# Kernel tuning notes

Hardware: AMD Instinct MI355X
Metric: run time of the kernel (lower is better)

The kernel has to match this reference:

```python
import math
import jax, jax.numpy as jnp
import numpy as np

NUM_HEADS = 8
EMBED_DIM = 512   # embed_dim_per_head(64) * num_heads(8)
LATENT = 256
HIDDEN = 512
INPUT_DIM = 128
P = 3             # function 'Q' -> 3 polynomial coefficients


def setup_inputs() -> dict:
    key = jax.random.key(0)
    ks = jax.random.split(key, 16)
    B, L, T, D, E = 64, 2048, 1024, INPUT_DIM, EMBED_DIM
    s = lambda fan_in: 1.0 / math.sqrt(fan_in)
    inp = {
        "timesteps": jax.random.uniform(ks[0], (B, L), jnp.float32),
        "X": jax.random.normal(ks[1], (B, L, D), jnp.float32),
        "M": jax.random.bernoulli(ks[2], 0.5, (B, L, D)).astype(jnp.float32),
        "y_time_steps": jax.random.uniform(ks[3], (B, T), jnp.float32),
        # time_embedding: Linear(1, E)
        "w_te": jax.random.normal(ks[4], (E,), jnp.float32),
        "b_te": jnp.zeros((E,), jnp.float32),
        # learned query [1, P, E]
        "query": jax.random.normal(ks[5], (1, P, E), jnp.float32),
        # query_map / key_map: Linear(E, E), stored [in, out]
        "W_q": jax.random.normal(ks[6], (E, E), jnp.float32) * s(E),
        "b_q": jnp.zeros((E,), jnp.float32),
        "W_k": jax.random.normal(ks[7], (E, E), jnp.float32) * s(E),
        "b_k": jnp.zeros((E,), jnp.float32),
        # attn out: Linear(2*D*H, latent)
        "W_o": jax.random.normal(ks[8], (2 * D * NUM_HEADS, LATENT), jnp.float32) * s(2 * D * NUM_HEADS),
        "b_o": jnp.zeros((LATENT,), jnp.float32),
        # decoder MLP: latent -> hidden -> hidden -> D
        "W1": jax.random.normal(ks[9], (LATENT, HIDDEN), jnp.float32) * s(LATENT),
        "b1": jnp.zeros((HIDDEN,), jnp.float32),
        "W2": jax.random.normal(ks[10], (HIDDEN, HIDDEN), jnp.float32) * s(HIDDEN),
        "b2": jnp.zeros((HIDDEN,), jnp.float32),
        "W3": jax.random.normal(ks[11], (HIDDEN, D), jnp.float32) * s(HIDDEN),
        "b3": jnp.zeros((D,), jnp.float32),
    }
    return inp


def _fld_forward(timesteps, X, M, y_time_steps, w_te, b_te, query,
                 W_q, b_q, W_k, b_k, W_o, b_o, W1, b1, W2, b2, W3, b3):
    B, L = timesteps.shape
    D = X.shape[-1]
    E, H = EMBED_DIM, NUM_HEADS
    ek = E // H
    # learn_time_embedding: Linear(1,E) then sin on indices range(0, E, H)
    key = timesteps[..., None] * w_te + b_te                      # [B,L,E]
    sin_mask = (jnp.arange(E) % H) == 0
    key = jnp.where(sin_mask, jnp.sin(key), key)
    Xcat = jnp.concatenate([X, M], axis=-1)                       # [B,L,2D]
    Mcat = jnp.concatenate([M, M], axis=-1)                       # [B,L,2D]
    # mask is used only for masked_fill in torch (no grad through it)
    maskb = jax.lax.stop_gradient((Mcat != 0).astype(Xcat.dtype))
    q = jnp.broadcast_to(query, (B, P, E)) @ W_q + b_q            # [B,P,E]
    k = key @ W_k + b_k                                            # [B,L,E]
    qh = q.reshape(B, P, H, ek).transpose(0, 2, 1, 3)             # [B,H,P,ek]
    kh = k.reshape(B, L, H, ek).transpose(0, 2, 1, 3)             # [B,H,L,ek]
    scores = jnp.einsum('bhpe,bhle->bhpl', qh, kh) / math.sqrt(ek)
    # per-channel masked softmax over L, factorized (masked entries -> exp(-1e9)=0)
    m = jnp.max(scores, axis=-1, keepdims=True)
    w = jnp.exp(scores - m)                                        # [B,H,P,L]
    num = jnp.einsum('bhpl,blc->bhpc', w, maskb * Xcat)            # [B,H,P,2D]
    den = jnp.einsum('bhpl,blc->bhpc', w, maskb)
    x = num / den                                                  # [B,H,P,2D]
    x = x.transpose(0, 2, 1, 3).reshape(B, P, H * 2 * D)
    coeffs = x @ W_o + b_o                                         # [B,P,latent]
    t = y_time_steps[..., None]                                    # [B,T,1]
    c0 = coeffs[:, 0:1, :]
    c1 = coeffs[:, 1:2, :]
    c2 = coeffs[:, 2:3, :]
    z = c0 + t * c1 + (t * t) * c2                                 # [B,T,latent]
    h1 = jax.nn.relu(z @ W1 + b1)
    h2 = jax.nn.relu(h1 @ W2 + b2)
    return h2 @ W3 + b3                                            # [B,T,D]


def reference(timesteps, X, M, y_time_steps, w_te, b_te, query,
              W_q, b_q, W_k, b_k, W_o, b_o, W1, b1, W2, b2, W3, b3):
    return _fld_forward(timesteps, X, M, y_time_steps, w_te, b_te, query,
                        W_q, b_q, W_k, b_k, W_o, b_o, W1, b1, W2, b2, W3, b3)
```

## Files before the change

### kernel.cpp

```cpp
#include <hip/hip_runtime.h>
#include <math.h>

#define NH   8
#define PP   3
#define HP   24
#define E    512
#define EK   64
#define D    128
#define LL   2048
#define BB   64
#define TT   1024
#define LAT  256
#define HID  512
#define CH2  16

typedef __attribute__((ext_vector_type(8))) short bf16x8;
typedef __attribute__((ext_vector_type(16))) float f32x16;

#define OFF_VS     ((size_t)2048)
#define OFF_WA     ((size_t)4096)
#define OFF_WB     ((size_t)4128)
#define OFF_SB     ((size_t)4160)
#define OFF_CVP    ((size_t)73728)
#define OFF_P2     ((size_t)81920)
#define OFF_PART   ((size_t)475136)
#define OFF_SC     ((size_t)3620864)
#define OFF_A      ((size_t)3784704)

__device__ inline ushort f2bf(float x) {
    union { float f; uint u; } v; v.f = x;
    uint r = v.u + 0x7fffu + ((v.u >> 16) & 1u);
    return (ushort)(r >> 16);
}
__device__ inline float bf2f(ushort u) {
    union { uint u; float f; } v; v.u = (uint)u << 16;
    return v.f;
}
__device__ inline uint swz(uint a)  { return a ^ (((a >> 8) & 7u) << 4); }
__device__ inline uint swzH(uint a) { return a ^ (((a >> 7) & 7u) << 4); }
__device__ inline uint pk2(float lo, float hi) {
    return (uint)f2bf(lo) | ((uint)f2bf(hi) << 16);
}
__device__ inline float h1f(float a0, float a1, float a2, float t) {
    return fmaxf(fmaf(t, fmaf(t, a2, a1), a0), 0.f);
}
__device__ inline int sigma(int s) { return s ^ (((((s >> 2) ^ (s >> 3)) & 1)) ? 12 : 0); }

__global__ __launch_bounds__(512) void k_setup(const float* __restrict__ query,
                                               const float* __restrict__ W_q,
                                               const float* __restrict__ b_q,
                                               const float* __restrict__ W_k,
                                               const float* __restrict__ b_k,
                                               const float* __restrict__ w_te,
                                               const float* __restrict__ b_te,
                                               const float* __restrict__ W_o,
                                               const float* __restrict__ W2,
                                               const float* __restrict__ W3,
                                               float* __restrict__ vsin,
                                               float* __restrict__ wA,
                                               float* __restrict__ wB,
                                               float* __restrict__ sbias,
                                               float* __restrict__ cvp,
                                               ushort* __restrict__ W2F,
                                               ushort* __restrict__ W3F) {
    int bx = blockIdx.x, tid = threadIdx.x;
    if (bx < HP) {
        int hp = bx, h = hp / PP, p = hp % PP;
        __shared__ float q_s[EK];
        __shared__ float qp[8][EK];
        {
            int e2 = tid & 63, ig = tid >> 6;
            float pacc = 0.f;
            const float* qr = query + p * E + ig * 64;
            const float* wq = W_q + (size_t)(ig * 64) * E + h * EK + e2;
            #pragma unroll 8
            for (int i = 0; i < 64; ++i)
                pacc = fmaf(qr[i], wq[(size_t)i * E], pacc);
            qp[ig][e2] = pacc;
        }
        __syncthreads();
        if (tid < EK) {
            float acc = b_q[h * EK + tid];
            #pragma unroll
            for (int g = 0; g < 8; ++g) acc += qp[g][tid];
            q_s[tid] = acc;
        }
        __syncthreads();
        int e = tid;
        const float scale = 0.125f;
        float acc = 0.f;
        {
            const float4* wk4 = (const float4*)(W_k + (size_t)e * E + h * EK);
            const float4* qs4 = (const float4*)q_s;
            #pragma unroll 4
            for (int j4 = 0; j4 < 16; ++j4) {
                float4 w4 = wk4[j4], q4 = qs4[j4];
                acc += w4.x * q4.x + w4.y * q4.y + w4.z * q4.z + w4.w * q4.w;
            }
        }
        float v = acc * scale;
        if ((e & 7) == 0) vsin[hp * 64 + (e >> 3)] = v;
        __shared__ float r1[512], r2[512];
        r1[e] = v * w_te[e];
        r2[e] = v * b_te[e];
        __syncthreads();
        for (int s = 256; s > 0; s >>= 1) {
            if (e < s) { r1[e] += r1[e + s]; r2[e] += r2[e + s]; }
            __syncthreads();
        }
        if (e == 0) {
            wA[hp] = r1[0];
            wB[hp] = r2[0];
            float sb = 0.f;
            for (int j = 0; j < EK; ++j) sb += b_k[h * EK + j] * q_s[j];
            sbias[hp] = sb * scale;
        }
    } else if (bx < HP + 32) {
        int bc = bx - HP;
        int h = bc >> 2, cc = bc & 3, o = tid & 255;
        float acc = 0.f;
        #pragma unroll 8
        for (int c = cc * 32; c < cc * 32 + 32; ++c)
            acc += W_o[(size_t)(h * 256 + 128 + c) * LAT + o];
        cvp[(h * 4 + cc) * LAT + o] = acc;
    } else {
        int gid = (bx - HP - 32) * 512 + tid;
        int l = gid & 63;
        int kb = 8 * (l >> 5);
        int cb = l & 31;
        if (gid < 32768) {
            int F = gid >> 6;
            int JT = F & 15, ks = F >> 4;
            int cbp = sigma(cb);
            int k0 = ks * 16 + kb, j = JT * 32 + cbp;
            #pragma unroll
            for (int e = 0; e < 8; ++e)
                W2F[(size_t)gid * 8 + e] = f2bf(W2[(size_t)(k0 + e) * HID + j]);
        } else {
            int g2 = gid - 32768;
            int F2 = g2 >> 6;
            int CT = F2 & 3, KT = F2 >> 2;
            int k0 = KT * 16 + kb, c = CT * 32 + cb;
            #pragma unroll
            for (int e = 0; e < 8; ++e)
                W3F[(size_t)g2 * 8 + e] = f2bf(W3[(size_t)(k0 + e) * D + c]);
        }
    }
}

__global__ __launch_bounds__(512, 8) void k_wsf2(const float* __restrict__ timesteps,
                                                 const float* __restrict__ w_te,
                                                 const float* __restrict__ b_te,
                                                 const float* __restrict__ vsin,
                                                 const float* __restrict__ wA,
                                                 const float* __restrict__ wB,
                                                 const float* __restrict__ sb,
                                                 const float* __restrict__ X,
                                                 const float* __restrict__ M,
                                                 ushort* __restrict__ part) {
    __shared__ char sbuf[40960];
    float* vs_s = (float*)sbuf;
    float* w8_s = (float*)(sbuf + 6144);
    float* b8_s = (float*)(sbuf + 6400);
    float* wA_s = (float*)(sbuf + 6656);
    float* wB_s = (float*)(sbuf + 6784);
    float* sb_s = (float*)(sbuf + 6912);
    ushort* vt  = (ushort*)sbuf;
    ushort* w_s = (ushort*)(sbuf + 32768);
    int b = blockIdx.x >> 4, ch = blockIdx.x & 15;
    int l0 = ch * 128;
    int tid = threadIdx.x;

    for (int i = tid; i < HP * 64; i += 512) vs_s[i] = vsin[i];
    if (tid < 64) { w8_s[tid] = w_te[tid * 8]; b8_s[tid] = b_te[tid * 8]; }
    if (tid < HP) { wA_s[tid] = wA[tid]; wB_s[tid] = wB[tid]; sb_s[tid] = sb[tid]; }
    __syncthreads();

    {
        int lpair = tid & 63, hh = tid >> 6;
        float ts0 = timesteps[(size_t)b * LL + l0 + lpair * 2];
        float ts1 = timesteps[(size_t)b * LL + l0 + lpair * 2 + 1];
        float sc0[3], sc1[3];
        #pragma unroll
        for (int i = 0; i < 3; ++i) {
            int hp = hh * 3 + i;
            sc0[i] = fmaf(ts0, wA_s[hp], wB_s[hp]) + sb_s[hp];
            sc1[i] = fmaf(ts1, wA_s[hp], wB_s[hp]) + sb_s[hp];
        }
        for (int jc = 0; jc < 64; jc += 8) {
            float d0[8], d1[8];
            #pragma unroll
            for (int j = 0; j < 8; ++j) {
                float w = w8_s[jc + j], bb = b8_s[jc + j];
                float k0 = fmaf(ts0, w, bb), k1 = fmaf(ts1, w, bb);
                d0[j] = __sinf(k0) - k0;
                d1[j] = __sinf(k1) - k1;
            }
            #pragma unroll
            for (int i = 0; i < 3; ++i) {
                int hp = hh * 3 + i;
                #pragma unroll
                for (int j = 0; j < 8; j += 4) {
                    float4 v4 = *(const float4*)&vs_s[hp * 64 + jc + j];
                    sc0[i] += d0[j] * v4.x + d0[j+1] * v4.y + d0[j+2] * v4.z + d0[j+3] * v4.w;
                    sc1[i] += d1[j] * v4.x + d1[j+1] * v4.y + d1[j+2] * v4.z + d1[j+3] * v4.w;
                }
            }
        }
        #pragma unroll
        for (int i = 0; i < 3; ++i) {
            int hp = hh * 3 + i;
            *(uint*)((char*)w_s + swz((uint)(hp * 256 + lpair * 4))) = pk2(__expf(sc0[i]), __expf(sc1[i]));
        }
        int hp = 24 + (tid >> 6), lp = tid & 63;
        *(uint*)((char*)w_s + swz((uint)(hp * 256 + lp * 4))) = 0u;
    }
    __syncthreads();

    int lane = tid & 63, wv = tid >> 6;
    int l31 = lane & 31, hl = lane >> 5;
    f32x16 acc;
    #pragma unroll
    for (int e = 0; e < 16; ++e) acc[e] = 0.f;

    int cst = tid & 127, lg = tid >> 7;
    for (int q = 0; q < 2; ++q) {
        if (q) __syncthreads();
        #pragma unroll
        for (int i = 0; i < 8; ++i) {
            int ll = lg * 16 + i * 2;
            size_t g0 = ((size_t)b * LL + l0 + q * 64 + ll) * D + cst;
            float m0 = M[g0], m1 = M[g0 + D];
            float x0 = X[g0] * m0, x1 = X[g0 + D] * m1;
            *(uint*)((char*)vt + swzH((uint)(cst * 128 + ll * 2)))         = pk2(x0, x1);
            *(uint*)((char*)vt + swzH((uint)((128 + cst) * 128 + ll * 2))) = pk2(m0, m1);
        }
        __syncthreads();
        #pragma unroll
        for (int ks = 0; ks < 4; ++ks) {
            bf16x8 af = *(const bf16x8*)((char*)w_s + swz((uint)(l31 * 256 + (q * 64 + ks * 16 + hl * 8) * 2)));
            bf16x8 bf_ = *(const bf16x8*)((char*)vt + swzH((uint)((wv * 32 + l31) * 128 + (ks * 16 + hl * 8) * 2)));
            acc = __builtin_amdgcn_mfma_f32_32x32x16_bf16(af, bf_, acc, 0, 0, 0);
        }
    }
    size_t base = ((size_t)(b * CH2 + ch) * HP) * 256;
    #pragma unroll
    for (int reg = 0; reg < 12; ++reg) {
        int hp = (reg & 3) + 8 * (reg >> 2) + 4 * hl;
        part[base + (size_t)hp * 256 + wv * 32 + l31] = f2bf(acc[reg]);
    }
}

__global__ __launch_bounds__(256) void k_mid(const ushort* __restrict__ part,
                                             const float* __restrict__ W_o,
                                             const float* __restrict__ cvp,
                                             const float* __restrict__ b_o,
                                             float* __restrict__ part2) {
    int bx = blockIdx.x, tid = threadIdx.x;
    int b = bx >> 3, h = bx & 7;
    __shared__ float ratio[PP][D];
    for (int ii = tid; ii < PP * D; ii += 256) {
        int p = ii >> 7, c = ii & 127;
        int hp = h * PP + p;
        float n = 0.f, d = 0.f;
        for (int ch = 0; ch < CH2; ++ch) {
            size_t base = ((size_t)(b * CH2 + ch) * HP + hp) * 256;
            n += bf2f(part[base + c]);
            d += bf2f(part[base + 128 + c]);
        }
        ratio[p][c] = n / d;
    }
    __syncthreads();
    int o = tid;
    float a0 = 0.f, a1 = 0.f, a2 = 0.f;
    #pragma unroll 4
    for (int c = 0; c < D; ++c) {
        float w = W_o[(size_t)(h * 256 + c) * LAT + o];
        a0 = fmaf(ratio[0][c], w, a0);
        a1 = fmaf(ratio[1][c], w, a1);
        a2 = fmaf(ratio[2][c], w, a2);
    }
    if (h == 0) {
        float cv = b_o[o];
        #pragma unroll 8
        for (int i = 0; i < 32; ++i) cv += cvp[i * LAT + o];
        a0 += cv; a1 += cv; a2 += cv;
    }
    size_t base = (((size_t)b * NH + h) * PP) * LAT + o;
    part2[base]           = a0;
    part2[base + LAT]     = a1;
    part2[base + 2 * LAT] = a2;
}

__global__ __launch_bounds__(128) void k_avec4(const float* __restrict__ part2,
                                               const float* __restrict__ W1,
                                               const float* __restrict__ b1,
                                               float* __restrict__ abuf) {
    int b = blockIdx.x, jq = blockIdx.y, tid = threadIdx.x;
    __shared__ float cf[PP * LAT];
    for (int idx = tid; idx < PP * LAT; idx += 128) {
        int p = idx / LAT, o = idx % LAT;
        float s = 0.f;
        #pragma unroll
        for (int h = 0; h < NH; ++h)
            s += part2[(((size_t)b * NH + h) * PP + p) * LAT + o];
        cf[p * LAT + o] = s;
    }
    __syncthreads();
    int j = jq * 128 + tid;
    float a0 = b1[j], a1 = 0.f, a2 = 0.f;
    #pragma unroll 4
    for (int k = 0; k < LAT; ++k) {
        float w = W1[(size_t)k * HID + j];
        a0 = fmaf(cf[k], w, a0);
        a1 = fmaf(cf[LAT + k], w, a1);
        a2 = fmaf(cf[2 * LAT + k], w, a2);
    }
    abuf[(size_t)b * 3 * HID + j] = a0;
    abuf[(size_t)b * 3 * HID + HID + j] = a1;
    abuf[(size_t)b * 3 * HID + 2 * HID + j] = a2;
}

__global__ __launch_bounds__(512, 4) void k_mlp12(const float* __restrict__ abuf,
                                                  const float* __restrict__ yts,
                                                  const ushort* __restrict__ W2F,
                                                  const float* __restrict__ b2,
                                                  const ushort* __restrict__ W3F,
                                                  const float* __restrict__ b3,
                                                  float* __restrict__ out) {
    __shared__ char lds[65536];
    int b = blockIdx.x, t0 = blockIdx.y * 64, tid = threadIdx.x;
    const float* a0p = abuf + (size_t)b * 3 * HID;
    const float* a1p = a0p + HID;
    const float* a2p = a1p + HID;

    {
        int sr = tid & 63, sub0 = (tid >> 6) & 1, skp = tid >> 7;
        float t = yts[(size_t)b * TT + t0 + sr];
        int kg0 = skp * 128 + sub0 * 64;
        uint sbase = (uint)(skp * 16384 + sr * 256 + sub0 * 128);
        #pragma unroll
        for (int i = 0; i < 8; ++i) {
            int k = kg0 + i * 8;
            float4 xa0 = *(const float4*)(a0p + k), xb0 = *(const float4*)(a0p + k + 4);
            float4 xa1 = *(const float4*)(a1p + k), xb1 = *(const float4*)(a1p + k + 4);
            float4 xa2 = *(const float4*)(a2p + k), xb2 = *(const float4*)(a2p + k + 4);
            uint4 pk;
            pk.x = pk2(h1f(xa0.x, xa1.x, xa2.x, t), h1f(xa0.y, xa1.y, xa2.y, t));
            pk.y = pk2(h1f(xa0.z, xa1.z, xa2.z, t), h1f(xa0.w, xa1.w, xa2.w, t));
            pk.z = pk2(h1f(xb0.x, xb1.x, xb2.x, t), h1f(xb0.y, xb1.y, xb2.y, t));
            pk.w = pk2(h1f(xb0.z, xb1.z, xb2.z, t), h1f(xb0.w, xb1.w, xb2.w, t));
            *(uint4*)(lds + swz(sbase + i * 16)) = pk;
        }
    }
    __syncthreads();

    int lane = tid & 63, w = tid >> 6;
    int l31 = lane & 31, hl = lane >> 5;
    int wp = w & 1, gw = w >> 1;
    int Jb = gw * 4 + wp * 2;

    f32x16 acc[2][2];
    #pragma unroll
    for (int jt = 0; jt < 2; ++jt) {
        int jT = (Jb + jt) * 32;
        #pragma unroll
        for (int reg = 0; reg < 16; ++reg) {
            int slot = (reg & 3) + 8 * (reg >> 2) + 4 * hl;
            float bv = b2[jT + sigma(slot)];
            acc[jt][0][reg] = bv;
            acc[jt][1][reg] = bv;
        }
    }
    #pragma unroll 4
    for (int ks = 0; ks < 32; ++ks) {
        uint base = (uint)((ks >> 3) * 16384 + (ks & 7) * 32 + hl * 16);
        bf16x8 bh0 = *(const bf16x8*)(lds + swz(base + (uint)(l31 * 256)));
        bf16x8 bh1 = *(const bf16x8*)(lds + swz(base + (uint)((32 + l31) * 256)));
        #pragma unroll
        for (int jt = 0; jt < 2; ++jt) {
            bf16x8 af = *(const bf16x8*)(W2F + ((size_t)(ks * 16 + Jb + jt) * 64 + lane) * 8);
            acc[jt][0] = __builtin_amdgcn_mfma_f32_32x32x16_bf16(af, bh0, acc[jt][0], 0, 0, 0);
            acc[jt][1] = __builtin_amdgcn_mfma_f32_32x32x16_bf16(af, bh1, acc[jt][1], 0, 0, 0);
        }
    }
    __syncthreads();

    #pragma unroll
    for (int jt = 0; jt < 2; ++jt) {
        int J = Jb + jt;
        #pragma unroll
        for (int rtile = 0; rtile < 2; ++rtile)
            #pragma unroll
            for (int s = 0; s < 2; ++s) {
                uint4 uu;
                uu.x = pk2(fmaxf(acc[jt][rtile][8 * s + 0], 0.f), fmaxf(acc[jt][rtile][8 * s + 1], 0.f));
                uu.y = pk2(fmaxf(acc[jt][rtile][8 * s + 2], 0.f), fmaxf(acc[jt][rtile][8 * s + 3], 0.f));
                uu.z = pk2(fmaxf(acc[jt][rtile][8 * s + 4], 0.f), fmaxf(acc[jt][rtile][8 * s + 5], 0.f));
                uu.w = pk2(fmaxf(acc[jt][rtile][8 * s + 6], 0.f), fmaxf(acc[jt][rtile][8 * s + 7], 0.f));
                *(uint4*)(lds + (uint)((rtile * 32 + J * 2 + s) * 1024 + lane * 16)) = uu;
            }
    }
    __syncthreads();

    f32x16 acc2a, acc2b;
    {
        float bv = b3[gw * 32 + l31];
        #pragma unroll
        for (int e = 0; e < 16; ++e) { acc2a[e] = bv; acc2b[e] = 0.f; }
    }
    #pragma unroll 4
    for (int sg = 0; sg < 32; sg += 2) {
        {
            bf16x8 ah = *(const bf16x8*)(lds + (uint)((wp * 32 + sg) * 1024 + lane * 16));
            bf16x8 bw = *(const bf16x8*)(W3F + ((size_t)(sg * 4 + gw) * 64 + lane) * 8);
            acc2a = __builtin_amdgcn_mfma_f32_32x32x16_bf16(ah, bw, acc2a, 0, 0, 0);
        }
        {
            bf16x8 ah = *(const bf16x8*)(lds + (uint)((wp * 32 + sg + 1) * 1024 + lane * 16));
            bf16x8 bw = *(const bf16x8*)(W3F + ((size_t)((sg + 1) * 4 + gw) * 64 + lane) * 8);
            acc2b = __builtin_amdgcn_mfma_f32_32x32x16_bf16(ah, bw, acc2b, 0, 0, 0);
        }
    }

    {
        int c = gw * 32 + l31;
        size_t rowbase = (size_t)b * TT + t0 + wp * 32 + 4 * hl;
        #pragma unroll
        for (int reg = 0; reg < 16; ++reg)
            out[(rowbase + (reg & 3) + 8 * (reg >> 2)) * D + c] = acc2a[reg] + acc2b[reg];
    }
}

extern "C" void kernel_launch(void* const* d_in, const int* in_sizes, int n_in,
                              void* d_out, int out_size, void* d_ws, size_t ws_size,
                              hipStream_t stream) {
    const float* timesteps = (const float*)d_in[0];
    const float* X        = (const float*)d_in[1];
    const float* M        = (const float*)d_in[2];
    const float* yts      = (const float*)d_in[3];
    const float* w_te     = (const float*)d_in[4];
    const float* b_te     = (const float*)d_in[5];
    const float* query    = (const float*)d_in[6];
    const float* W_q      = (const float*)d_in[7];
    const float* b_q      = (const float*)d_in[8];
    const float* W_k      = (const float*)d_in[9];
    const float* b_k      = (const float*)d_in[10];
    const float* W_o      = (const float*)d_in[11];
    const float* b_o      = (const float*)d_in[12];
    const float* W1       = (const float*)d_in[13];
    const float* b1       = (const float*)d_in[14];
    const float* W2       = (const float*)d_in[15];
    const float* b2       = (const float*)d_in[16];
    const float* W3       = (const float*)d_in[17];
    const float* b3       = (const float*)d_in[18];
    float* out = (float*)d_out;
    float* ws  = (float*)d_ws;

    float* vsin   = ws + OFF_VS;
    float* wA     = ws + OFF_WA;
    float* wB     = ws + OFF_WB;
    float* sbias  = ws + OFF_SB;
    float* cvp    = ws + OFF_CVP;
    float* part2  = ws + OFF_P2;
    ushort* part  = (ushort*)(ws + OFF_PART);
    float* abuf   = ws + OFF_A;
    ushort* W2F   = (ushort*)(ws + OFF_SC);
    ushort* W3F   = W2F + (size_t)HID * HID;

    hipLaunchKernelGGL(k_setup,  dim3(HP + 32 + 80),  dim3(512), 0, stream,
                       query, W_q, b_q, W_k, b_k, w_te, b_te, W_o, W2, W3,
                       vsin, wA, wB, sbias, cvp, W2F, W3F);
    hipLaunchKernelGGL(k_wsf2,   dim3(BB * CH2),      dim3(512), 0, stream,
                       timesteps, w_te, b_te, vsin, wA, wB, sbias, X, M, part);
    hipLaunchKernelGGL(k_mid,    dim3(BB * NH),       dim3(256), 0, stream,
                       part, W_o, cvp, b_o, part2);
    hipLaunchKernelGGL(k_avec4,  dim3(BB, 4),         dim3(128), 0, stream,
                       part2, W1, b1, abuf);
    hipLaunchKernelGGL(k_mlp12,  dim3(BB, TT / 64),   dim3(512), 0, stream,
                       abuf, yts, W2F, b2, W3F, b3, out);
}
```

Baseline: 134.8 us.

## Halve MLP row tile to 32 rows and split layer-3 K across waves

The fused MLP kernel now processes 32 time rows per block instead of 64, which halves shared memory to 32KB and doubles the grid so more blocks can be resident. Layer 3 is reorganised so the eight waves split the K dimension into two halves with an LDS reduction, instead of each wave holding two accumulators. The cost is that each W2/W3 fragment is loaded from global memory twice as often per output row, plus an extra sync and LDS round trip for the reduction.

```diff
diff --git a/kernel.cpp b/kernel.cpp
--- a/kernel.cpp
+++ b/kernel.cpp
@@ -321,27 +321,28 @@
     abuf[(size_t)b * 3 * HID + 2 * HID + j] = a2;
 }
 
-__global__ __launch_bounds__(512, 4) void k_mlp12(const float* __restrict__ abuf,
+__global__ __launch_bounds__(512, 4) void k_mlp32(const float* __restrict__ abuf,
                                                   const float* __restrict__ yts,
                                                   const ushort* __restrict__ W2F,
                                                   const float* __restrict__ b2,
                                                   const ushort* __restrict__ W3F,
                                                   const float* __restrict__ b3,
                                                   float* __restrict__ out) {
-    __shared__ char lds[65536];
-    int b = blockIdx.x, t0 = blockIdx.y * 64, tid = threadIdx.x;
+    __shared__ char lds[32768];
+    int b = blockIdx.x, t0 = blockIdx.y * 32, tid = threadIdx.x;
     const float* a0p = abuf + (size_t)b * 3 * HID;
     const float* a1p = a0p + HID;
     const float* a2p = a1p + HID;
 
     {
-        int sr = tid & 63, sub0 = (tid >> 6) & 1, skp = tid >> 7;
+        int sr = tid & 31, kblk = tid >> 5;
+        int kp = kblk >> 2, ksub = kblk & 3;
         float t = yts[(size_t)b * TT + t0 + sr];
-        int kg0 = skp * 128 + sub0 * 64;
-        uint sbase = (uint)(skp * 16384 + sr * 256 + sub0 * 128);
-        #pragma unroll
-        for (int i = 0; i < 8; ++i) {
-            int k = kg0 + i * 8;
+        int k0 = kp * 128 + ksub * 32;
+        uint sbase = (uint)(kp * 8192 + sr * 256 + ksub * 64);
+        #pragma unroll
+        for (int i = 0; i < 4; ++i) {
+            int k = k0 + i * 8;
             float4 xa0 = *(const float4*)(a0p + k), xb0 = *(const float4*)(a0p + k + 4);
             float4 xa1 = *(const float4*)(a1p + k), xb1 = *(const float4*)(a1p + k + 4);
             float4 xa2 = *(const float4*)(a2p + k), xb2 = *(const float4*)(a2p + k + 4);
@@ -357,78 +358,79 @@
 
     int lane = tid & 63, w = tid >> 6;
     int l31 = lane & 31, hl = lane >> 5;
-    int wp = w & 1, gw = w >> 1;
-    int Jb = gw * 4 + wp * 2;
-
-    f32x16 acc[2][2];
+    int J0 = w * 2;
+
+    f32x16 acc[2];
     #pragma unroll
     for (int jt = 0; jt < 2; ++jt) {
-        int jT = (Jb + jt) * 32;
+        int jT = (J0 + jt) * 32;
         #pragma unroll
         for (int reg = 0; reg < 16; ++reg) {
             int slot = (reg & 3) + 8 * (reg >> 2) + 4 * hl;
-            float bv = b2[jT + sigma(slot)];
-            acc[jt][0][reg] = bv;
-            acc[jt][1][reg] = bv;
+            acc[jt][reg] = b2[jT + sigma(slot)];
         }
     }
     #pragma unroll 4
     for (int ks = 0; ks < 32; ++ks) {
-        uint base = (uint)((ks >> 3) * 16384 + (ks & 7) * 32 + hl * 16);
-        bf16x8 bh0 = *(const bf16x8*)(lds + swz(base + (uint)(l31 * 256)));
-        bf16x8 bh1 = *(const bf16x8*)(lds + swz(base + (uint)((32 + l31) * 256)));
+        uint base = (uint)((ks >> 3) * 8192 + l31 * 256 + (ks & 7) * 32 + hl * 16);
+        bf16x8 bh = *(const bf16x8*)(lds + swz(base));
         #pragma unroll
         for (int jt = 0; jt < 2; ++jt) {
-            bf16x8 af = *(const bf16x8*)(W2F + ((size_t)(ks * 16 + Jb + jt) * 64 + lane) * 8);
-            acc[jt][0] = __builtin_amdgcn_mfma_f32_32x32x16_bf16(af, bh0, acc[jt][0], 0, 0, 0);
-            acc[jt][1] = __builtin_amdgcn_mfma_f32_32x32x16_bf16(af, bh1, acc[jt][1], 0, 0, 0);
+            bf16x8 af = *(const bf16x8*)(W2F + ((size_t)(ks * 16 + J0 + jt) * 64 + lane) * 8);
+            acc[jt] = __builtin_amdgcn_mfma_f32_32x32x16_bf16(af, bh, acc[jt], 0, 0, 0);
         }
     }
     __syncthreads();
 
     #pragma unroll
     for (int jt = 0; jt < 2; ++jt) {
-        int J = Jb + jt;
-        #pragma unroll
-        for (int rtile = 0; rtile < 2; ++rtile)
-            #pragma unroll
-            for (int s = 0; s < 2; ++s) {
-                uint4 uu;
-                uu.x = pk2(fmaxf(acc[jt][rtile][8 * s + 0], 0.f), fmaxf(acc[jt][rtile][8 * s + 1], 0.f));
-                uu.y = pk2(fmaxf(acc[jt][rtile][8 * s + 2], 0.f), fmaxf(acc[jt][rtile][8 * s + 3], 0.f));
-                uu.z = pk2(fmaxf(acc[jt][rtile][8 * s + 4], 0.f), fmaxf(acc[jt][rtile][8 * s + 5], 0.f));
-                uu.w = pk2(fmaxf(acc[jt][rtile][8 * s + 6], 0.f), fmaxf(acc[jt][rtile][8 * s + 7], 0.f));
-                *(uint4*)(lds + (uint)((rtile * 32 + J * 2 + s) * 1024 + lane * 16)) = uu;
-            }
-    }
-    __syncthreads();
-
-    f32x16 acc2a, acc2b;
+        int J = J0 + jt;
+        #pragma unroll
+        for (int s = 0; s < 2; ++s) {
+            uint4 uu;
+            uu.x = pk2(fmaxf(acc[jt][8 * s + 0], 0.f), fmaxf(acc[jt][8 * s + 1], 0.f));
+            uu.y = pk2(fmaxf(acc[jt][8 * s + 2], 0.f), fmaxf(acc[jt][8 * s + 3], 0.f));
+            uu.z = pk2(fmaxf(acc[jt][8 * s + 4], 0.f), fmaxf(acc[jt][8 * s + 5], 0.f));
+            uu.w = pk2(fmaxf(acc[jt][8 * s + 6], 0.f), fmaxf(acc[jt][8 * s + 7], 0.f));
+            *(uint4*)(lds + (uint)((J * 2 + s) * 1024 + lane * 16)) = uu;
+        }
+    }
+    __syncthreads();
+
+    int ct = w & 3, kh = w >> 2;
+    f32x16 acc2;
     {
-        float bv = b3[gw * 32 + l31];
-        #pragma unroll
-        for (int e = 0; e < 16; ++e) { acc2a[e] = bv; acc2b[e] = 0.f; }
+        float bv = (kh == 0) ? b3[ct * 32 + l31] : 0.f;
+        #pragma unroll
+        for (int e = 0; e < 16; ++e) acc2[e] = bv;
     }
     #pragma unroll 4
-    for (int sg = 0; sg < 32; sg += 2) {
-        {
-            bf16x8 ah = *(const bf16x8*)(lds + (uint)((wp * 32 + sg) * 1024 + lane * 16));
-            bf16x8 bw = *(const bf16x8*)(W3F + ((size_t)(sg * 4 + gw) * 64 + lane) * 8);
-            acc2a = __builtin_amdgcn_mfma_f32_32x32x16_bf16(ah, bw, acc2a, 0, 0, 0);
-        }
-        {
-            bf16x8 ah = *(const bf16x8*)(lds + (uint)((wp * 32 + sg + 1) * 1024 + lane * 16));
-            bf16x8 bw = *(const bf16x8*)(W3F + ((size_t)((sg + 1) * 4 + gw) * 64 + lane) * 8);
-            acc2b = __builtin_amdgcn_mfma_f32_32x32x16_bf16(ah, bw, acc2b, 0, 0, 0);
-        }
-    }
-
-    {
-        int c = gw * 32 + l31;
-        size_t rowbase = (size_t)b * TT + t0 + wp * 32 + 4 * hl;
-        #pragma unroll
-        for (int reg = 0; reg < 16; ++reg)
-            out[(rowbase + (reg & 3) + 8 * (reg >> 2)) * D + c] = acc2a[reg] + acc2b[reg];
+    for (int u = 0; u < 16; ++u) {
+        int sg = kh * 16 + u;
+        bf16x8 ah = *(const bf16x8*)(lds + (uint)(sg * 1024 + lane * 16));
+        bf16x8 bw = *(const bf16x8*)(W3F + ((size_t)(sg * 4 + ct) * 64 + lane) * 8);
+        acc2 = __builtin_amdgcn_mfma_f32_32x32x16_bf16(ah, bw, acc2, 0, 0, 0);
+    }
+    __syncthreads();
+
+    float* red = (float*)lds;
+    if (kh == 1) {
+        #pragma unroll
+        for (int reg = 0; reg < 16; ++reg) {
+            int rloc = (reg & 3) + 8 * (reg >> 2) + 4 * hl;
+            red[ct * 1024 + rloc * 32 + l31] = acc2[reg];
+        }
+    }
+    __syncthreads();
+    if (kh == 0) {
+        int c = ct * 32 + l31;
+        size_t rowbase = (size_t)b * TT + t0;
+        #pragma unroll
+        for (int reg = 0; reg < 16; ++reg) {
+            int rloc = (reg & 3) + 8 * (reg >> 2) + 4 * hl;
+            float v = acc2[reg] + red[ct * 1024 + rloc * 32 + l31];
+            out[(rowbase + rloc) * D + c] = v;
+        }
     }
 }
 
@@ -477,6 +479,6 @@
                        part, W_o, cvp, b_o, part2);
     hipLaunchKernelGGL(k_avec4,  dim3(BB, 4),         dim3(128), 0, stream,
                        part2, W1, b1, abuf);
-    hipLaunchKernelGGL(k_mlp12,  dim3(BB, TT / 64),   dim3(512), 0, stream,
+    hipLaunchKernelGGL(k_mlp32,  dim3(BB, TT / 32),   dim3(512), 0, stream,
                        abuf, yts, W2F, b2, W3F, b3, out);
 }
```

Result: slower. 146.9 us (+9.0%).
